# Kernel tuning notes

Hardware: AMD Instinct MI355X
Metric: run time of the kernel (lower is better)

## Reference

```python
import jax, jax.numpy as jnp
import numpy as np

T, B = 2048, 128
H = 128          # hidden_size
QH = 1024        # query_hidden_size
NF = 32          # num_convolution_filters
K = 31           # convolution_filter_size (odd, same padding)


def setup_inputs() -> dict:
    key = jax.random.key(0)
    ks = jax.random.split(key, 10)
    encoded_tokens = jax.random.normal(ks[0], (T, B, H), dtype=jnp.float32)
    tokens_mask = jax.random.randint(ks[1], (B, T), 0, 2).astype(jnp.bool_)
    query = jax.random.normal(ks[2], (1, B, QH), dtype=jnp.float32)
    cumulative_alignment = jax.random.uniform(ks[3], (B, T), dtype=jnp.float32)
    # parameters
    conv_w = jax.random.normal(ks[4], (NF, 1, K), dtype=jnp.float32) * 0.1   # Conv1d weight [out,in,k]
    conv_b = jnp.zeros((NF,), dtype=jnp.float32)
    Wq = jax.random.normal(ks[5], (H, QH), dtype=jnp.float32) * (1.0 / np.sqrt(QH))
    bq = jnp.zeros((H,), dtype=jnp.float32)
    Wa = jax.random.normal(ks[6], (H, NF), dtype=jnp.float32) * (1.0 / np.sqrt(NF))
    ba = jnp.zeros((H,), dtype=jnp.float32)
    score_w = jax.random.normal(ks[7], (H,), dtype=jnp.float32) * (1.0 / np.sqrt(H))  # xavier-ish
    score_b = jnp.zeros((H,), dtype=jnp.float32)
    return dict(encoded_tokens=encoded_tokens, tokens_mask=tokens_mask, query=query,
                cumulative_alignment=cumulative_alignment, conv_w=conv_w, conv_b=conv_b,
                Wq=Wq, bq=bq, Wa=Wa, ba=ba, score_w=score_w, score_b=score_b)


def reference(encoded_tokens, tokens_mask, query, cumulative_alignment,
              conv_w, conv_b, Wq, bq, Wa, ba, score_w, score_b):
    # location features: Conv1d over cumulative alignment, same padding
    loc = jax.lax.conv_general_dilated(
        cumulative_alignment[:, None, :], conv_w,
        window_strides=(1,), padding=[((K - 1) // 2, (K - 1) // 2)],
        dimension_numbers=('NCH', 'OIH', 'NCH'))  # [B, NF, T]
    loc = loc + conv_b[None, :, None]
    loc = jnp.transpose(loc, (2, 0, 1))                        # [T, B, NF]
    loc = jnp.einsum('tbf,hf->tbh', loc, Wa) + ba              # [T, B, H]
    q = jnp.einsum('obq,hq->obh', query, Wq) + bq              # [1, B, H]
    # additive score: tanh of fused elementwise sum, then project to scalar
    score = jnp.tanh(encoded_tokens + q + loc + score_b)       # [T, B, H]
    s = jnp.einsum('tbh,h->bt', score, score_w)                # [B, T]
    s = jnp.where(tokens_mask, -jnp.inf, s)
    alignment = jax.nn.softmax(s, axis=1)                      # [B, T]
    context = jnp.einsum('bt,tbh->bh', alignment, encoded_tokens)  # [B, H]
    cumulative_alignment = cumulative_alignment + alignment
    return context, cumulative_alignment, alignment
```

## Files before the change

### kernel.cpp

```cpp
#include <hip/hip_runtime.h>
#include <stdint.h>

#define T_DIM 2048
#define B_DIM 128
#define H_DIM 128
#define QH_DIM 1024
#define NF 32
#define KW 31
#define TB 128
#define NTILE (T_DIM / TB)
#define CPAD_ROW (T_DIM + 32)

#define NEG_INF (-__builtin_inff())

typedef float v2f __attribute__((ext_vector_type(2)));

__device__ __forceinline__ float fast_tanh(float x) {
    float e = __expf(2.0f * x);
    return 1.0f - 2.0f * __builtin_amdgcn_rcpf(1.0f + e);
}

template <int C>
__device__ __forceinline__ float dpp_add(float x) {
    int m = __builtin_amdgcn_update_dpp(0, __float_as_int(x), C, 0xf, 0xf, true);
    return x + __int_as_float(m);
}
__device__ __forceinline__ float wave_sum64(float x) {
    x = dpp_add<0x111>(x); x = dpp_add<0x112>(x); x = dpp_add<0x114>(x); x = dpp_add<0x118>(x);
    x = dpp_add<0x142>(x); x = dpp_add<0x143>(x);
    return __int_as_float(__builtin_amdgcn_readlane(__float_as_int(x), 63));
}

__global__ __launch_bounds__(256)
void k_prep(const float* __restrict__ cum, const void* __restrict__ mask,
            float* __restrict__ cpad, float* __restrict__ mbias) {
    const int gid = blockIdx.x * 256 + threadIdx.x;
    const int b = gid >> 11, t = gid & 2047;
    const int l = threadIdx.x & 63;
    uint32_t u = ((const uint32_t*)mask)[l];
    unsigned long long hi = __ballot(u > 1u);
    unsigned long long nf = __ballot(u != 0u && u != 0x3f800000u);
    int layout = (hi == 0ull) ? 0 : ((nf == 0ull) ? 2 : 1);
    bool m;
    if (layout == 0)      m = ((const int32_t*)mask)[gid] != 0;
    else if (layout == 1) m = ((const uint8_t*)mask)[gid] != 0;
    else                  m = ((const float*)mask)[gid] != 0.0f;
    mbias[gid] = m ? NEG_INF : 0.0f;
    cpad[b * CPAD_ROW + 16 + t] = cum[gid];
    if (t < 16) cpad[b * CPAD_ROW + t] = 0.0f;
    else if (t >= T_DIM - 16) cpad[b * CPAD_ROW + 32 + t] = 0.0f;
}

__global__ void k0_G(const float* __restrict__ Wa, const float* __restrict__ conv_w,
                     float* __restrict__ Gt) {
    int gid = blockIdx.x * blockDim.x + threadIdx.x;
    if (gid >= KW * H_DIM) return;
    int k = gid >> 7, h = gid & 127;
    float acc = 0.0f;
    #pragma unroll
    for (int f = 0; f < NF; ++f) acc = fmaf(Wa[h * NF + f], conv_w[f * KW + k], acc);
    Gt[gid] = acc;
}

__global__ __launch_bounds__(512)
void k1_query(const float* __restrict__ query, const float* __restrict__ Wq,
              const float* __restrict__ bq, const float* __restrict__ Wa,
              const float* __restrict__ conv_b, const float* __restrict__ ba,
              const float* __restrict__ score_b, float* __restrict__ qb) {
    const int b = blockIdx.x, tid = threadIdx.x;
    const int h = tid & 127, qtr = tid >> 7;
    __shared__ __align__(16) float qrow[QH_DIM];
    __shared__ float partial[512];
    for (int i = tid; i < QH_DIM; i += 512) qrow[i] = query[b * QH_DIM + i];
    __syncthreads();
    const float4* wq4 = (const float4*)(Wq + (size_t)h * QH_DIM + qtr * 256);
    const float4* q4 = (const float4*)(qrow + qtr * 256);
    float acc = 0.0f;
    #pragma unroll 4
    for (int j = 0; j < 64; ++j) {
        float4 w = wq4[j], q = q4[j];
        acc += w.x * q.x + w.y * q.y + w.z * q.z + w.w * q.w;
    }
    if (qtr == 0) {
        float cb = bq[h] + ba[h] + score_b[h];
        #pragma unroll
        for (int f = 0; f < NF; ++f) cb = fmaf(Wa[h * NF + f], conv_b[f], cb);
        acc += cb;
    }
    partial[tid] = acc;
    __syncthreads();
    if (tid < 128) qb[b * H_DIM + h] = partial[h] + partial[h + 128] + partial[h + 256] + partial[h + 384];
}

__global__ __launch_bounds__(256, 2)
void k2_fused(const float* __restrict__ enc, const float* __restrict__ cpad,
              const float* __restrict__ mbias, const float* __restrict__ Gt,
              const float* __restrict__ qb, const float* __restrict__ score_w,
              float* __restrict__ s_out, float* __restrict__ o_part,
              float* __restrict__ ml_part) {
    const int b = blockIdx.x;
    const int tl = blockIdx.y;
    const int tid = threadIdx.x;
    const int l = tid & 63;
    const int wv = __builtin_amdgcn_readfirstlane(tid >> 6);
    const int tw0 = tl * TB + wv * 32;

    __shared__ float oc[4][H_DIM];
    __shared__ float mwl[4], lwl[4];

    v2f G[KW];
    #pragma unroll
    for (int k = 0; k < KW; ++k) G[k] = *(const v2f*)(Gt + k * H_DIM + 2 * l);

    const v2f base = *(const v2f*)(qb + b * H_DIM + 2 * l);
    const v2f w2 = *(const v2f*)(score_w + 2 * l);
    const float* crow = cpad + b * CPAD_ROW;
    const float* mrow = mbias + b * T_DIM;

    float m_w = NEG_INF, l_w = 0.0f;
    v2f o = {0.0f, 0.0f};
    float sv = 0.0f;

    #pragma unroll
    for (int c = 0; c < 4; ++c) {
        const int tb = tw0 + c * 8;

        float sc[38];
        #pragma unroll
        for (int j = 0; j < 38; ++j) sc[j] = crow[tb + 1 + j];

        v2f ee[8];
        #pragma unroll
        for (int it = 0; it < 8; ++it)
            ee[it] = *(const v2f*)(enc + ((size_t)(tb + it) * B_DIM + b) * H_DIM + 2 * l);

        float su[8];
        #pragma unroll
        for (int it = 0; it < 8; ++it) {
            v2f acc = base;
            #pragma unroll
            for (int k = 0; k < KW; ++k)
                acc = __builtin_elementwise_fma(G[k], (v2f){sc[it + k], sc[it + k]}, acc);
            const v2f a2 = acc + ee[it];
            float p = w2.x * fast_tanh(a2.x) + w2.y * fast_tanh(a2.y);
            su[it] = wave_sum64(p) + mrow[tb + it];
        }

        #pragma unroll
        for (int it = 0; it < 8; ++it) sv = (l == c * 8 + it) ? su[it] : sv;

        float m8 = su[0];
        #pragma unroll
        for (int it = 1; it < 8; ++it) m8 = fmaxf(m8, su[it]);
        const float m_new = fmaxf(m_w, m8);
        const float m_use = (m_new == NEG_INF) ? 0.0f : m_new;
        const float alpha = __expf(m_w - m_use);
        float lsum = 0.0f;
        v2f osum = {0.0f, 0.0f};
        #pragma unroll
        for (int it = 0; it < 8; ++it) {
            const float e = __expf(su[it] - m_use);
            lsum += e;
            osum = __builtin_elementwise_fma((v2f){e, e}, ee[it], osum);
        }
        l_w = fmaf(l_w, alpha, lsum);
        o = __builtin_elementwise_fma(o, (v2f){alpha, alpha}, osum);
        m_w = m_new;
    }

    if (l < 32) s_out[b * T_DIM + tw0 + l] = sv;

    oc[wv][2 * l] = o.x;
    oc[wv][2 * l + 1] = o.y;
    if (l == 0) { mwl[wv] = m_w; lwl[wv] = l_w; }
    __syncthreads();
    if (tid < H_DIM) {
        const float mb = fmaxf(fmaxf(mwl[0], mwl[1]), fmaxf(mwl[2], mwl[3]));
        const float mu = (mb == NEG_INF) ? 0.0f : mb;
        const float b0 = __expf(mwl[0] - mu), b1 = __expf(mwl[1] - mu);
        const float b2 = __expf(mwl[2] - mu), b3 = __expf(mwl[3] - mu);
        const float ov = oc[0][tid] * b0 + oc[1][tid] * b1 + oc[2][tid] * b2 + oc[3][tid] * b3;
        const int tbase = b * NTILE + tl;
        o_part[tbase * H_DIM + tid] = ov;
        if (tid == 0) {
            ml_part[tbase * 2] = mb;
            ml_part[tbase * 2 + 1] = lwl[0] * b0 + lwl[1] * b1 + lwl[2] * b2 + lwl[3] * b3;
        }
    }
}

__global__ __launch_bounds__(256)
void k5_final(float* __restrict__ s_align, const float* __restrict__ cum_in,
              float* __restrict__ cum_out, const float* __restrict__ o_part,
              const float* __restrict__ ml_part, float* __restrict__ ctx) {
    const int b = blockIdx.x, tid = threadIdx.x;
    __shared__ float sm[NTILE], sl[NTILE], sb[NTILE];
    if (tid < NTILE) {
        sm[tid] = ml_part[(b * NTILE + tid) * 2];
        sl[tid] = ml_part[(b * NTILE + tid) * 2 + 1];
    }
    __syncthreads();
    float M = sm[0];
    #pragma unroll
    for (int i = 1; i < NTILE; ++i) M = fmaxf(M, sm[i]);
    const float M_use = (M == NEG_INF) ? 0.0f : M;
    if (tid < NTILE) sb[tid] = __expf(sm[tid] - M_use);
    __syncthreads();
    float L = 0.0f;
    #pragma unroll
    for (int i = 0; i < NTILE; ++i) L = fmaf(sl[i], sb[i], L);
    const float invL = 1.0f / L;
    if (tid < H_DIM) {
        float ov = 0.0f;
        #pragma unroll
        for (int i = 0; i < NTILE; ++i)
            ov = fmaf(o_part[(b * NTILE + i) * H_DIM + tid], sb[i], ov);
        ctx[b * H_DIM + tid] = ov * invL;
    }
    #pragma unroll
    for (int j = 0; j < 8; ++j) {
        const int idx = b * T_DIM + tid + j * 256;
        const float a = __expf(s_align[idx] - M_use) * invL;
        s_align[idx] = a;
        cum_out[idx] = cum_in[idx] + a;
    }
}

extern "C" void kernel_launch(void* const* d_in, const int* in_sizes, int n_in,
                              void* d_out, int out_size, void* d_ws, size_t ws_size,
                              hipStream_t stream) {
    const float* enc     = (const float*)d_in[0];
    const void*  mask    = d_in[1];
    const float* query   = (const float*)d_in[2];
    const float* cum     = (const float*)d_in[3];
    const float* conv_w  = (const float*)d_in[4];
    const float* conv_b  = (const float*)d_in[5];
    const float* Wq      = (const float*)d_in[6];
    const float* bq      = (const float*)d_in[7];
    const float* Wa      = (const float*)d_in[8];
    const float* ba      = (const float*)d_in[9];
    const float* score_w = (const float*)d_in[10];
    const float* score_b = (const float*)d_in[11];

    float* ctx_out   = (float*)d_out;
    float* cum_out   = ctx_out + B_DIM * H_DIM;
    float* align_out = cum_out + B_DIM * T_DIM;

    float* Gt     = (float*)d_ws;
    float* qb     = Gt + 4096;
    float* o_part = qb + B_DIM * H_DIM;
    float* ml     = o_part + B_DIM * NTILE * H_DIM;
    float* cpad   = ml + 8192;
    float* mb     = cpad + B_DIM * CPAD_ROW;

    k_prep<<<B_DIM * T_DIM / 256, 256, 0, stream>>>(cum, mask, cpad, mb);
    k0_G<<<16, 256, 0, stream>>>(Wa, conv_w, Gt);
    k1_query<<<B_DIM, 512, 0, stream>>>(query, Wq, bq, Wa, conv_b, ba, score_b, qb);
    k2_fused<<<dim3(B_DIM, NTILE), 256, 0, stream>>>(enc, cpad, mb, Gt, qb, score_w,
                                                     align_out, o_part, ml);
    k5_final<<<B_DIM, 256, 0, stream>>>(align_out, cum, cum_out, o_part, ml, ctx_out);
}
```

Before: 242.7 us.

## Merge prep kernels into one launch and fold final reduction via last-block atomic

Combines the mask/cum prep, conv-weight fold, and query projection kernels into a single launch whose blocks are partitioned by block index. The final softmax normalization and context combine move into the fused score kernel, where the last tile block per batch row (found with an atomic counter and threadfences) does the merge. This cuts five launches to two and removes launch gaps. In exchange it adds atomics and fences to every block and a serialized tail in the last block per row.

```diff
diff --git a/kernel.cpp b/kernel.cpp
--- a/kernel.cpp
+++ b/kernel.cpp
@@ -11,6 +11,9 @@
 #define NTILE (T_DIM / TB)
 #define CPAD_ROW (T_DIM + 32)
 
+#define PREP_NB 512
+#define G_NB 8
+
 #define NEG_INF (-__builtin_inff())
 
 typedef float v2f __attribute__((ext_vector_type(2)));
@@ -31,73 +34,80 @@
     return __int_as_float(__builtin_amdgcn_readlane(__float_as_int(x), 63));
 }
 
-__global__ __launch_bounds__(256)
-void k_prep(const float* __restrict__ cum, const void* __restrict__ mask,
-            float* __restrict__ cpad, float* __restrict__ mbias) {
-    const int gid = blockIdx.x * 256 + threadIdx.x;
-    const int b = gid >> 11, t = gid & 2047;
-    const int l = threadIdx.x & 63;
-    uint32_t u = ((const uint32_t*)mask)[l];
-    unsigned long long hi = __ballot(u > 1u);
-    unsigned long long nf = __ballot(u != 0u && u != 0x3f800000u);
-    int layout = (hi == 0ull) ? 0 : ((nf == 0ull) ? 2 : 1);
-    bool m;
-    if (layout == 0)      m = ((const int32_t*)mask)[gid] != 0;
-    else if (layout == 1) m = ((const uint8_t*)mask)[gid] != 0;
-    else                  m = ((const float*)mask)[gid] != 0.0f;
-    mbias[gid] = m ? NEG_INF : 0.0f;
-    cpad[b * CPAD_ROW + 16 + t] = cum[gid];
-    if (t < 16) cpad[b * CPAD_ROW + t] = 0.0f;
-    else if (t >= T_DIM - 16) cpad[b * CPAD_ROW + 32 + t] = 0.0f;
-}
-
-__global__ void k0_G(const float* __restrict__ Wa, const float* __restrict__ conv_w,
-                     float* __restrict__ Gt) {
-    int gid = blockIdx.x * blockDim.x + threadIdx.x;
-    if (gid >= KW * H_DIM) return;
-    int k = gid >> 7, h = gid & 127;
-    float acc = 0.0f;
-    #pragma unroll
-    for (int f = 0; f < NF; ++f) acc = fmaf(Wa[h * NF + f], conv_w[f * KW + k], acc);
-    Gt[gid] = acc;
-}
-
 __global__ __launch_bounds__(512)
-void k1_query(const float* __restrict__ query, const float* __restrict__ Wq,
-              const float* __restrict__ bq, const float* __restrict__ Wa,
-              const float* __restrict__ conv_b, const float* __restrict__ ba,
-              const float* __restrict__ score_b, float* __restrict__ qb) {
-    const int b = blockIdx.x, tid = threadIdx.x;
-    const int h = tid & 127, qtr = tid >> 7;
-    __shared__ __align__(16) float qrow[QH_DIM];
-    __shared__ float partial[512];
-    for (int i = tid; i < QH_DIM; i += 512) qrow[i] = query[b * QH_DIM + i];
-    __syncthreads();
-    const float4* wq4 = (const float4*)(Wq + (size_t)h * QH_DIM + qtr * 256);
-    const float4* q4 = (const float4*)(qrow + qtr * 256);
-    float acc = 0.0f;
-    #pragma unroll 4
-    for (int j = 0; j < 64; ++j) {
-        float4 w = wq4[j], q = q4[j];
-        acc += w.x * q.x + w.y * q.y + w.z * q.z + w.w * q.w;
-    }
-    if (qtr == 0) {
-        float cb = bq[h] + ba[h] + score_b[h];
-        #pragma unroll
-        for (int f = 0; f < NF; ++f) cb = fmaf(Wa[h * NF + f], conv_b[f], cb);
-        acc += cb;
-    }
-    partial[tid] = acc;
-    __syncthreads();
-    if (tid < 128) qb[b * H_DIM + h] = partial[h] + partial[h + 128] + partial[h + 256] + partial[h + 384];
+void kA_prep(const float* __restrict__ cum, const void* __restrict__ mask,
+             float* __restrict__ cpad, float* __restrict__ mbias,
+             const float* __restrict__ Wa, const float* __restrict__ conv_w,
+             float* __restrict__ Gt,
+             const float* __restrict__ query, const float* __restrict__ Wq,
+             const float* __restrict__ bq, const float* __restrict__ conv_b,
+             const float* __restrict__ ba, const float* __restrict__ score_b,
+             float* __restrict__ qb, int* __restrict__ cnt) {
+    const int bid = blockIdx.x;
+    const int tid = threadIdx.x;
+
+    if (bid < PREP_NB) {
+        const int gid = bid * 512 + tid;
+        const int b = gid >> 11, t = gid & 2047;
+        const int l = tid & 63;
+        uint32_t u = ((const uint32_t*)mask)[l];
+        unsigned long long hi = __ballot(u > 1u);
+        unsigned long long nf = __ballot(u != 0u && u != 0x3f800000u);
+        int layout = (hi == 0ull) ? 0 : ((nf == 0ull) ? 2 : 1);
+        bool m;
+        if (layout == 0)      m = ((const int32_t*)mask)[gid] != 0;
+        else if (layout == 1) m = ((const uint8_t*)mask)[gid] != 0;
+        else                  m = ((const float*)mask)[gid] != 0.0f;
+        mbias[gid] = m ? NEG_INF : 0.0f;
+        cpad[b * CPAD_ROW + 16 + t] = cum[gid];
+        if (t < 16) cpad[b * CPAD_ROW + t] = 0.0f;
+        else if (t >= T_DIM - 16) cpad[b * CPAD_ROW + 32 + t] = 0.0f;
+        if (gid < B_DIM) cnt[gid] = 0;
+    } else if (bid < PREP_NB + G_NB) {
+        const int gid = (bid - PREP_NB) * 512 + tid;
+        if (gid < KW * H_DIM) {
+            const int k = gid >> 7, h = gid & 127;
+            float acc = 0.0f;
+            #pragma unroll
+            for (int f = 0; f < NF; ++f) acc = fmaf(Wa[h * NF + f], conv_w[f * KW + k], acc);
+            Gt[gid] = acc;
+        }
+    } else {
+        const int b = bid - (PREP_NB + G_NB);
+        const int h = tid & 127, qtr = tid >> 7;
+        __shared__ __align__(16) float qrow[QH_DIM];
+        __shared__ float partial[512];
+        for (int i = tid; i < QH_DIM; i += 512) qrow[i] = query[b * QH_DIM + i];
+        __syncthreads();
+        const float4* wq4 = (const float4*)(Wq + (size_t)h * QH_DIM + qtr * 256);
+        const float4* q4 = (const float4*)(qrow + qtr * 256);
+        float acc = 0.0f;
+        #pragma unroll 4
+        for (int j = 0; j < 64; ++j) {
+            float4 w = wq4[j], q = q4[j];
+            acc += w.x * q.x + w.y * q.y + w.z * q.z + w.w * q.w;
+        }
+        if (qtr == 0) {
+            float cb = bq[h] + ba[h] + score_b[h];
+            #pragma unroll
+            for (int f = 0; f < NF; ++f) cb = fmaf(Wa[h * NF + f], conv_b[f], cb);
+            acc += cb;
+        }
+        partial[tid] = acc;
+        __syncthreads();
+        if (tid < 128)
+            qb[b * H_DIM + h] = partial[h] + partial[h + 128] + partial[h + 256] + partial[h + 384];
+    }
 }
 
 __global__ __launch_bounds__(256, 2)
-void k2_fused(const float* __restrict__ enc, const float* __restrict__ cpad,
+void kB_fused(const float* __restrict__ enc, const float* __restrict__ cpad,
               const float* __restrict__ mbias, const float* __restrict__ Gt,
               const float* __restrict__ qb, const float* __restrict__ score_w,
-              float* __restrict__ s_out, float* __restrict__ o_part,
-              float* __restrict__ ml_part) {
+              float* __restrict__ s_align, float* __restrict__ o_part,
+              float* __restrict__ ml_part,
+              const float* __restrict__ cum_in, float* __restrict__ cum_out,
+              float* __restrict__ ctx, int* __restrict__ cnt) {
     const int b = blockIdx.x;
     const int tl = blockIdx.y;
     const int tid = threadIdx.x;
@@ -107,6 +117,7 @@
 
     __shared__ float oc[4][H_DIM];
     __shared__ float mwl[4], lwl[4];
+    __shared__ int lastFlag;
 
     v2f G[KW];
     #pragma unroll
@@ -168,7 +179,7 @@
         m_w = m_new;
     }
 
-    if (l < 32) s_out[b * T_DIM + tw0 + l] = sv;
+    if (l < 32) s_align[b * T_DIM + tw0 + l] = sv;
 
     oc[wv][2 * l] = o.x;
     oc[wv][2 * l + 1] = o.y;
@@ -187,34 +198,35 @@
             ml_part[tbase * 2 + 1] = lwl[0] * b0 + lwl[1] * b1 + lwl[2] * b2 + lwl[3] * b3;
         }
     }
-}
-
-__global__ __launch_bounds__(256)
-void k5_final(float* __restrict__ s_align, const float* __restrict__ cum_in,
-              float* __restrict__ cum_out, const float* __restrict__ o_part,
-              const float* __restrict__ ml_part, float* __restrict__ ctx) {
-    const int b = blockIdx.x, tid = threadIdx.x;
-    __shared__ float sm[NTILE], sl[NTILE], sb[NTILE];
+
+    __threadfence();
+    __syncthreads();
+    if (tid == 0) lastFlag = (atomicAdd(&cnt[b], 1) == NTILE - 1);
+    __syncthreads();
+    if (!lastFlag) return;
+    __threadfence();
+
+    __shared__ float fm[NTILE], fl[NTILE], fb[NTILE];
     if (tid < NTILE) {
-        sm[tid] = ml_part[(b * NTILE + tid) * 2];
-        sl[tid] = ml_part[(b * NTILE + tid) * 2 + 1];
-    }
-    __syncthreads();
-    float M = sm[0];
-    #pragma unroll
-    for (int i = 1; i < NTILE; ++i) M = fmaxf(M, sm[i]);
+        fm[tid] = ml_part[(b * NTILE + tid) * 2];
+        fl[tid] = ml_part[(b * NTILE + tid) * 2 + 1];
+    }
+    __syncthreads();
+    float M = fm[0];
+    #pragma unroll
+    for (int i = 1; i < NTILE; ++i) M = fmaxf(M, fm[i]);
     const float M_use = (M == NEG_INF) ? 0.0f : M;
-    if (tid < NTILE) sb[tid] = __expf(sm[tid] - M_use);
+    if (tid < NTILE) fb[tid] = __expf(fm[tid] - M_use);
     __syncthreads();
     float L = 0.0f;
     #pragma unroll
-    for (int i = 0; i < NTILE; ++i) L = fmaf(sl[i], sb[i], L);
+    for (int i = 0; i < NTILE; ++i) L = fmaf(fl[i], fb[i], L);
     const float invL = 1.0f / L;
     if (tid < H_DIM) {
         float ov = 0.0f;
         #pragma unroll
         for (int i = 0; i < NTILE; ++i)
-            ov = fmaf(o_part[(b * NTILE + i) * H_DIM + tid], sb[i], ov);
+            ov = fmaf(o_part[(b * NTILE + i) * H_DIM + tid], fb[i], ov);
         ctx[b * H_DIM + tid] = ov * invL;
     }
     #pragma unroll
@@ -252,11 +264,12 @@
     float* ml     = o_part + B_DIM * NTILE * H_DIM;
     float* cpad   = ml + 8192;
     float* mb     = cpad + B_DIM * CPAD_ROW;
-
-    k_prep<<<B_DIM * T_DIM / 256, 256, 0, stream>>>(cum, mask, cpad, mb);
-    k0_G<<<16, 256, 0, stream>>>(Wa, conv_w, Gt);
-    k1_query<<<B_DIM, 512, 0, stream>>>(query, Wq, bq, Wa, conv_b, ba, score_b, qb);
-    k2_fused<<<dim3(B_DIM, NTILE), 256, 0, stream>>>(enc, cpad, mb, Gt, qb, score_w,
-                                                     align_out, o_part, ml);
-    k5_final<<<B_DIM, 256, 0, stream>>>(align_out, cum, cum_out, o_part, ml, ctx_out);
-}
+    int*   cnt    = (int*)(mb + B_DIM * T_DIM);
+
+    kA_prep<<<PREP_NB + G_NB + B_DIM, 512, 0, stream>>>(
+        cum, mask, cpad, mb, Wa, conv_w, Gt,
+        query, Wq, bq, conv_b, ba, score_b, qb, cnt);
+    kB_fused<<<dim3(B_DIM, NTILE), 256, 0, stream>>>(
+        enc, cpad, mb, Gt, qb, score_w,
+        align_out, o_part, ml, cum, cum_out, ctx_out, cnt);
+}
```

Result: slower. 516.0 us (+112.7%).
